# Kernel tuning notes

Hardware: AMD Instinct MI355X
Metric: run time of the kernel (lower is better)

The kernel has to match this reference:

```python
import jax, jax.numpy as jnp
import numpy as np

N_NODES = 100000
HEADS = 4
HEAD_DIM = 32  # hidden_channels // heads
NEG_SLOPE = 0.2


def gat_layer(x, W, a_src, a_dst, b, src, dst):
    # x: [N, Fin], W: [Fin, H*C], a_src/a_dst: [H, C], b: [H*C]
    N = x.shape[0]
    h = (x @ W).reshape(N, HEADS, HEAD_DIM)            # [N, H, C]
    alpha_s = jnp.einsum('nhc,hc->nh', h, a_src)       # [N, H]
    alpha_d = jnp.einsum('nhc,hc->nh', h, a_dst)       # [N, H]
    e = jax.nn.leaky_relu(alpha_s[src] + alpha_d[dst], NEG_SLOPE)  # [E, H]
    # segment softmax over edges grouped by destination node
    e_max = jax.ops.segment_max(e, dst, num_segments=N)           # [N, H]
    ex = jnp.exp(e - e_max[dst])                                   # [E, H]
    denom = jax.ops.segment_sum(ex, dst, num_segments=N)          # [N, H]
    alpha = ex / denom[dst]                                        # [E, H]
    msg = h[src] * alpha[:, :, None]                               # [E, H, C]
    out = jax.ops.segment_sum(msg, dst, num_segments=N)           # [N, H, C]
    return out.reshape(N, HEADS * HEAD_DIM) + b


def setup_inputs() -> dict:
    key = jax.random.key(0)
    ks = jax.random.split(key, 10)
    Fin, H, C = 128, HEADS, HEAD_DIM
    x = jax.random.normal(ks[0], (N_NODES, Fin), dtype=jnp.float32)
    edge_index = jax.random.randint(ks[1], (2, 1000000), 0, N_NODES, dtype=jnp.int64)
    s = 1.0 / np.sqrt(Fin)
    W1 = jax.random.normal(ks[2], (Fin, H * C), dtype=jnp.float32) * s
    a_src1 = jax.random.normal(ks[3], (H, C), dtype=jnp.float32) * 0.1
    a_dst1 = jax.random.normal(ks[4], (H, C), dtype=jnp.float32) * 0.1
    b1 = jnp.zeros((H * C,), dtype=jnp.float32)
    s2 = 1.0 / np.sqrt(H * C)
    W2 = jax.random.normal(ks[5], (H * C, H * C), dtype=jnp.float32) * s2
    a_src2 = jax.random.normal(ks[6], (H, C), dtype=jnp.float32) * 0.1
    a_dst2 = jax.random.normal(ks[7], (H, C), dtype=jnp.float32) * 0.1
    b2 = jnp.zeros((H * C,), dtype=jnp.float32)
    return {"x": x, "edge_index": edge_index, "W1": W1, "a_src1": a_src1,
            "a_dst1": a_dst1, "b1": b1, "W2": W2, "a_src2": a_src2,
            "a_dst2": a_dst2, "b2": b2}


def reference(x, edge_index, W1, a_src1, a_dst1, b1, W2, a_src2, a_dst2, b2):
    N = x.shape[0]
    # add self-loops (PyG add_self_loops=True)
    loop = jnp.arange(N, dtype=edge_index.dtype)
    src = jnp.concatenate([edge_index[0], loop])
    dst = jnp.concatenate([edge_index[1], loop])
    h = gat_layer(x, W1, a_src1, a_dst1, b1, src, dst)
    h = jax.nn.elu(h)
    h = gat_layer(h, W2, a_src2, a_dst2, b2, src, dst)
    h = jax.nn.elu(h)
    return h
```

## Files before the change

kernel.cpp:

```cpp
#include <hip/hip_runtime.h>
#include <math.h>

#define NHEADS 4
#define HDIM 32
#define F 128
#define ACH 8192

typedef __attribute__((ext_vector_type(8))) short bf16x8;
typedef __attribute__((ext_vector_type(4))) float f32x4;
typedef __attribute__((ext_vector_type(4))) unsigned u32x4;

__device__ __forceinline__ float lrelu(float v) { return v > 0.f ? v : 0.2f * v; }

__device__ __forceinline__ unsigned short cvt_bf16(float f) {
    unsigned u = __float_as_uint(f);
    u += 0x7fffu + ((u >> 16) & 1u);
    return (unsigned short)(u >> 16);
}

__global__ void k_packW2(const float* __restrict__ W1, const float* __restrict__ as1,
                         const float* __restrict__ ad1, const float* __restrict__ W2,
                         const float* __restrict__ as2, const float* __restrict__ ad2,
                         short* __restrict__ Wb) {
    int idx = blockIdx.x * 256 + threadIdx.x;
    if (idx >= 2 * 36 * 512) return;
    int half = idx >= 36 * 512;
    const float* W     = half ? W2 : W1;
    const float* a_src = half ? as2 : as1;
    const float* a_dst = half ? ad2 : ad1;
    int r = idx - half * 36 * 512;
    int j    = r & 7;
    int lane = (r >> 3) & 63;
    int frag = r >> 9;
    int kk = frag / 9, ct = frag % 9;
    int k = kk * 32 + (lane >> 4) * 8 + j;
    int col = lane & 15;
    float val;
    if (ct < 8) {
        val = W[k * F + ct * 16 + col];
    } else if (col < 8) {
        int head = col & 3;
        const float* av = (col < 4) ? a_src : a_dst;
        float sum = 0.f;
        #pragma unroll 8
        for (int c = 0; c < HDIM; ++c)
            sum += W[k * F + head * HDIM + c] * av[head * HDIM + c];
        val = sum;
    } else {
        val = 0.f;
    }
    Wb[idx] = (short)cvt_bf16(val);
}

template<bool ABF16>
__global__ __launch_bounds__(256) void k_gemm_mfma(
    const void* __restrict__ xv, const short* __restrict__ Wb,
    unsigned short* __restrict__ hbf, float* __restrict__ as_out,
    float* __restrict__ ad_out, int N)
{
    const int wid  = threadIdx.x >> 6;
    const int lane = threadIdx.x & 63;
    const int rowbase = blockIdx.x * 64 + wid * 16;
    const int row  = rowbase + (lane & 15);
    const int rowc = min(row, N - 1);
    const int col = lane & 15;

    f32x4 acc[9] = {};
    #pragma unroll
    for (int kk = 0; kk < 4; ++kk) {
        bf16x8 a;
        if constexpr (ABF16) {
            const unsigned short* xr =
                (const unsigned short*)xv + (size_t)rowc * F + (lane >> 4) * 8;
            a = *(const bf16x8*)(xr + kk * 32);
        } else {
            const float* xr = (const float*)xv + (size_t)rowc * F + (lane >> 4) * 8;
            float4 xa = *(const float4*)(xr + kk * 32);
            float4 xb = *(const float4*)(xr + kk * 32 + 4);
            a[0] = cvt_bf16(xa.x); a[1] = cvt_bf16(xa.y);
            a[2] = cvt_bf16(xa.z); a[3] = cvt_bf16(xa.w);
            a[4] = cvt_bf16(xb.x); a[5] = cvt_bf16(xb.y);
            a[6] = cvt_bf16(xb.z); a[7] = cvt_bf16(xb.w);
        }
        const bf16x8* bp = (const bf16x8*)(Wb + (size_t)(kk * 9) * 512 + lane * 8);
        #pragma unroll
        for (int ct = 0; ct < 9; ++ct) {
            bf16x8 b = bp[ct * 64];
            acc[ct] = __builtin_amdgcn_mfma_f32_16x16x32_bf16(a, b, acc[ct], 0, 0, 0);
        }
    }

    const int r0 = rowbase + (lane >> 4) * 4;
    #pragma unroll
    for (int i = 0; i < 4; ++i) {
        int r = r0 + i;
        if (r < N) {
            #pragma unroll
            for (int ct = 0; ct < 8; ++ct)
                __builtin_nontemporal_store(cvt_bf16(acc[ct][i]),
                                            &hbf[(size_t)r * F + ct * 16 + col]);
            if (col < 4)       as_out[r * NHEADS + col]     = acc[8][i];
            else if (col < 8)  ad_out[r * NHEADS + col - 4] = acc[8][i];
        }
    }
}


__global__ __launch_bounds__(512) void k_bhist(
    const int* __restrict__ src, const int* __restrict__ dst,
    int* __restrict__ bha, int nbuc, int E, int TOT)
{
    __shared__ int hist[512];
    int t = threadIdx.x;
    hist[t] = 0;
    __syncthreads();
    int base = blockIdx.x * ACH;
    for (int k = 0; k < ACH / 512; ++k) {
        int i = base + k * 512 + t;
        if (i < TOT) {
            int d = (i < E) ? dst[i] : (i - E);
            atomicAdd(&hist[d >> 8], 1);
        }
    }
    __syncthreads();
    if (t < nbuc) bha[(size_t)blockIdx.x * nbuc + t] = hist[t];
}

__global__ __launch_bounds__(256) void k_bscan1(
    int* __restrict__ bha, int* __restrict__ btot, int nbuc, int nab)
{
    int t = blockIdx.x * 256 + threadIdx.x;
    if (t >= nbuc) return;
    int run = 0;
    int j = 0;
    for (; j + 4 <= nab; j += 4) {
        int v0 = bha[(size_t)(j + 0) * nbuc + t];
        int v1 = bha[(size_t)(j + 1) * nbuc + t];
        int v2 = bha[(size_t)(j + 2) * nbuc + t];
        int v3 = bha[(size_t)(j + 3) * nbuc + t];
        bha[(size_t)(j + 0) * nbuc + t] = run; run += v0;
        bha[(size_t)(j + 1) * nbuc + t] = run; run += v1;
        bha[(size_t)(j + 2) * nbuc + t] = run; run += v2;
        bha[(size_t)(j + 3) * nbuc + t] = run; run += v3;
    }
    for (; j < nab; ++j) {
        int v = bha[(size_t)j * nbuc + t];
        bha[(size_t)j * nbuc + t] = run; run += v;
    }
    btot[t] = run;
}

__global__ __launch_bounds__(512) void k_bscan2(
    const int* __restrict__ btot, int* __restrict__ bbase, int nbuc)
{
    __shared__ int sh[512];
    int t = threadIdx.x;
    int v = (t < nbuc) ? btot[t] : 0;
    sh[t] = v;
    __syncthreads();
    for (int off = 1; off < 512; off <<= 1) {
        int u = (t >= off) ? sh[t - off] : 0;
        __syncthreads();
        sh[t] += u;
        __syncthreads();
    }
    if (t < nbuc) {
        bbase[t] = sh[t] - v;
        if (t == nbuc - 1) bbase[nbuc] = sh[t];
    }
}

__global__ __launch_bounds__(256) void k_bscan3(
    int* __restrict__ bha, const int* __restrict__ bbase, int nbuc, int total)
{
    int i = blockIdx.x * 256 + threadIdx.x;
    if (i < total) bha[i] += bbase[i % nbuc];
}

__global__ __launch_bounds__(512) void k_bscatter(
    const int* __restrict__ src, const int* __restrict__ dst,
    const int* __restrict__ bha, unsigned* __restrict__ epack,
    int nbuc, int E, int TOT)
{
    __shared__ int cur[512];
    int t = threadIdx.x;
    cur[t] = (t < nbuc) ? bha[(size_t)blockIdx.x * nbuc + t] : 0;
    __syncthreads();
    int base = blockIdx.x * ACH;
    for (int k = 0; k < ACH / 512; ++k) {
        int i = base + k * 512 + t;
        if (i < TOT) {
            int s, d;
            if (i < E) { s = src[i]; d = dst[i]; } else { s = d = i - E; }
            int pos = atomicAdd(&cur[d >> 8], 1);
            epack[pos] = ((unsigned)s << 8) | (unsigned)(d & 255);
        }
    }
}

__global__ __launch_bounds__(256) void k_bfinal(
    const unsigned* __restrict__ epack, const int* __restrict__ bbase,
    int* __restrict__ deg, int* __restrict__ rowptr, int* __restrict__ ssrc,
    int* __restrict__ bh, int N, int nbuc)
{
    __shared__ int hist[256];
    __shared__ int sh[256];
    __shared__ int cur[256];
    int t = threadIdx.x;
    hist[t] = 0;
    __syncthreads();
    int s0 = bbase[blockIdx.x], s1 = bbase[blockIdx.x + 1];
    for (int i = s0 + t; i < s1; i += 256)
        atomicAdd(&hist[epack[i] & 255u], 1);
    __syncthreads();
    int h = hist[t];
    sh[t] = h;
    __syncthreads();
    for (int off = 1; off < 256; off <<= 1) {
        int u = (t >= off) ? sh[t - off] : 0;
        __syncthreads();
        sh[t] += u;
        __syncthreads();
    }
    int node = blockIdx.x * 256 + t;
    int excl = s0 + sh[t] - h;
    cur[t] = excl;
    if (node < N) {
        deg[node] = h;
        rowptr[node] = excl;
        atomicAdd(&bh[(blockIdx.x >> 2) * 256 + min(h, 255)], 1);
    }
    if (node == 0) rowptr[N] = bbase[nbuc];
    __syncthreads();
    for (int i = s0 + t; i < s1; i += 256) {
        unsigned p = epack[i];
        int pos = atomicAdd(&cur[p & 255u], 1);
        ssrc[pos] = (int)(p >> 8);
    }
}

__global__ __launch_bounds__(256) void k_sort_off(int* __restrict__ bh, int nb)
{
    int t = threadIdx.x;
    int run = 0;
    for (int j = 0; j < nb; ++j) {
        int v = bh[j * 256 + t];
        bh[j * 256 + t] = run;
        run += v;
    }
    __shared__ int sh[256];
    int tot = run;
    sh[t] = tot;
    __syncthreads();
    for (int off = 1; off < 256; off <<= 1) {
        int u = (t >= off) ? sh[t - off] : 0;
        __syncthreads();
        sh[t] += u;
        __syncthreads();
    }
    int bucket_base = sh[t] - tot;
    for (int j = 0; j < nb; ++j)
        bh[j * 256 + t] += bucket_base;
}

__global__ __launch_bounds__(256) void k_sort_scatter(
    const int* __restrict__ deg, const int* __restrict__ bh,
    const int* __restrict__ rowptr, int4* __restrict__ ninfo, int N)
{
    __shared__ int cur[256];
    int t = threadIdx.x;
    cur[t] = bh[blockIdx.x * 256 + t];
    __syncthreads();
    int base = blockIdx.x * 1024;
    #pragma unroll
    for (int g = 0; g < 4; ++g) {
        int i = base + g * 256 + t;
        if (i < N) {
            int pos = atomicAdd(&cur[min(deg[i], 255)], 1);
            ninfo[pos] = make_int4(rowptr[i], rowptr[i + 1], i, 0);
        }
    }
}

template<bool OUTBF16>
__global__ __launch_bounds__(256) void k_aggregate(
    const int4* __restrict__ ninfo, const int* __restrict__ ssrc,
    const float* __restrict__ as, const float* __restrict__ ad,
    const unsigned short* __restrict__ hbf, const float* __restrict__ bias,
    void* __restrict__ outv, int N)
{
    int gi = (blockIdx.x * 256 + threadIdx.x) >> 4;
    if (gi >= N) return;
    const int4 ni   = ninfo[gi];
    const int start = ni.x, end = ni.y, node = ni.z;
    const int l16   = threadIdx.x & 15;
    const int hb    = l16 >> 2;
    const int c0    = l16 * 8;
    const float adB = ad[node * NHEADS + hb];

    float a0=0.f,a1=0.f,a2=0.f,a3=0.f,a4=0.f,a5=0.f,a6=0.f,a7=0.f;
    float dacc = 0.f;
    for (int base = start; base < end; base += 8) {
        int   sj[8];
        float fj[8];
        uint4 hj[8];
        #pragma unroll
        for (int j = 0; j < 8; ++j)
            sj[j] = ssrc[min(base + j, end - 1)];
        #pragma unroll
        for (int j = 0; j < 8; ++j)
            fj[j] = as[sj[j] * NHEADS + hb];
        #pragma unroll
        for (int j = 0; j < 8; ++j)
            hj[j] = *(const uint4*)(hbf + (size_t)sj[j] * F + c0);
        #pragma unroll
        for (int j = 0; j < 8; ++j) {
            float ex = (base + j < end) ? __expf(lrelu(fj[j] + adB)) : 0.f;
            dacc += ex;
            a0 = fmaf(ex, __uint_as_float(hj[j].x << 16),         a0);
            a1 = fmaf(ex, __uint_as_float(hj[j].x & 0xffff0000u), a1);
            a2 = fmaf(ex, __uint_as_float(hj[j].y << 16),         a2);
            a3 = fmaf(ex, __uint_as_float(hj[j].y & 0xffff0000u), a3);
            a4 = fmaf(ex, __uint_as_float(hj[j].z << 16),         a4);
            a5 = fmaf(ex, __uint_as_float(hj[j].z & 0xffff0000u), a5);
            a6 = fmaf(ex, __uint_as_float(hj[j].w << 16),         a6);
            a7 = fmaf(ex, __uint_as_float(hj[j].w & 0xffff0000u), a7);
        }
    }
    float inv = 1.f / dacc;
    float v[8] = {a0,a1,a2,a3,a4,a5,a6,a7};
    #pragma unroll
    for (int k = 0; k < 8; ++k) {
        float t = v[k] * inv + bias[c0 + k];
        v[k] = t > 0.f ? t : expm1f(t);
    }
    if (OUTBF16) {
        u32x4 o;
        o.x = (unsigned)cvt_bf16(v[0]) | ((unsigned)cvt_bf16(v[1]) << 16);
        o.y = (unsigned)cvt_bf16(v[2]) | ((unsigned)cvt_bf16(v[3]) << 16);
        o.z = (unsigned)cvt_bf16(v[4]) | ((unsigned)cvt_bf16(v[5]) << 16);
        o.w = (unsigned)cvt_bf16(v[6]) | ((unsigned)cvt_bf16(v[7]) << 16);
        __builtin_nontemporal_store(o,
            (u32x4*)((unsigned short*)outv + (size_t)node * F + c0));
    } else {
        f32x4 o0 = {v[0], v[1], v[2], v[3]};
        f32x4 o1 = {v[4], v[5], v[6], v[7]};
        float* op = (float*)outv + (size_t)node * F + c0;
        __builtin_nontemporal_store(o0, (f32x4*)op);
        __builtin_nontemporal_store(o1, (f32x4*)(op + 4));
    }
}

extern "C" void kernel_launch(void* const* d_in, const int* in_sizes, int n_in,
                              void* d_out, int out_size, void* d_ws, size_t ws_size,
                              hipStream_t stream)
{
    const float* x      = (const float*)d_in[0];
    const int*   eidx   = (const int*)d_in[1];
    const float* W1     = (const float*)d_in[2];
    const float* a_src1 = (const float*)d_in[3];
    const float* a_dst1 = (const float*)d_in[4];
    const float* b1     = (const float*)d_in[5];
    const float* W2     = (const float*)d_in[6];
    const float* a_src2 = (const float*)d_in[7];
    const float* a_dst2 = (const float*)d_in[8];
    const float* b2     = (const float*)d_in[9];

    const int N = in_sizes[0] / F;
    const int E = in_sizes[1] / 2;
    const int TOT = E + N;
    const int* src = eidx;
    const int* dst = eidx + E;

    const int nbuc = (N + 255) / 256;
    const int nab  = (TOT + ACH - 1) / ACH;
    const int nb   = (N + 1023) / 1024;

    unsigned* epack = (unsigned*)d_ws;
    unsigned short* hbf    = (unsigned short*)(epack + TOT);
    unsigned short* out1bf = hbf + (size_t)N * F;
    float* as = (float*)(out1bf + (size_t)N * F);
    float* ad = as + (size_t)N * NHEADS;
    int* deg    = (int*)(ad + (size_t)N * NHEADS);
    int* rowptr = deg + N;
    int* ssrc   = rowptr + N + 1;
    int4* ninfo = (int4*)(((uintptr_t)(ssrc + TOT) + 15) & ~(uintptr_t)15);
    int* bh     = (int*)(ninfo + N);
    int* bha    = bh + (size_t)nb * 256;
    int* btot   = bha + (size_t)nab * nbuc;
    int* bbase  = btot + nbuc;
    short* Wb1  = (short*)(((uintptr_t)(bbase + nbuc + 1) + 15) & ~(uintptr_t)15);

    const int gemmBlocks = (N + 63) / 64;
    const int aggBlocks  = (N + 15) / 16;

    k_packW2<<<144, 256, 0, stream>>>(W1, a_src1, a_dst1, W2, a_src2, a_dst2, Wb1);
    short* Wb2 = Wb1 + 36 * 512;

    k_bhist<<<nab, 512, 0, stream>>>(src, dst, bha, nbuc, E, TOT);
    k_bscan1<<<(nbuc + 255) / 256, 256, 0, stream>>>(bha, btot, nbuc, nab);
    k_bscan2<<<1, 512, 0, stream>>>(btot, bbase, nbuc);
    k_bscan3<<<(nab * nbuc + 255) / 256, 256, 0, stream>>>(bha, bbase, nbuc, nab * nbuc);
    k_bscatter<<<nab, 512, 0, stream>>>(src, dst, bha, epack, nbuc, E, TOT);
    (void)hipMemsetAsync(bh, 0, (size_t)nb * 256 * sizeof(int), stream);
    k_bfinal<<<nbuc, 256, 0, stream>>>(epack, bbase, deg, rowptr, ssrc, bh, N, nbuc);

    k_sort_off<<<1, 256, 0, stream>>>(bh, nb);
    k_sort_scatter<<<nb, 256, 0, stream>>>(deg, bh, rowptr, ninfo, N);

    k_gemm_mfma<false><<<gemmBlocks, 256, 0, stream>>>(x, Wb1, hbf, as, ad, N);
    k_aggregate<true><<<aggBlocks, 256, 0, stream>>>(ninfo, ssrc, as, ad, hbf, b1, out1bf, N);

    k_gemm_mfma<true><<<gemmBlocks, 256, 0, stream>>>(out1bf, Wb2, hbf, as, ad, N);
    k_aggregate<false><<<aggBlocks, 256, 0, stream>>>(ninfo, ssrc, as, ad, hbf, b2, d_out, N);
}
```

Before: 266.9 us.

## Fold scan-add into scatter, pre-scale logits by log2e, widen serial scan unroll

Removes the k_bscan3 launch by adding the bucket base offsets inside k_bscatter when its shared cursors are initialized. Attention logits are pre-multiplied by log2(e) in the GEMM epilogue so the aggregate can use exp2f instead of __expf. LeakyReLU is positively homogeneous, so this scaling leaves the result mathematically unchanged. The serial column scans in k_bscan1 and k_sort_off now unroll by 8 to keep more loads in flight, which costs some extra register use.

```diff
diff --git a/kernel.cpp b/kernel.cpp
--- a/kernel.cpp
+++ b/kernel.cpp
@@ -5,6 +5,7 @@
 #define HDIM 32
 #define F 128
 #define ACH 8192
+#define LOG2E 1.44269504088896340736f
 
 typedef __attribute__((ext_vector_type(8))) short bf16x8;
 typedef __attribute__((ext_vector_type(4))) float f32x4;
@@ -99,8 +100,8 @@
             for (int ct = 0; ct < 8; ++ct)
                 __builtin_nontemporal_store(cvt_bf16(acc[ct][i]),
                                             &hbf[(size_t)r * F + ct * 16 + col]);
-            if (col < 4)       as_out[r * NHEADS + col]     = acc[8][i];
-            else if (col < 8)  ad_out[r * NHEADS + col - 4] = acc[8][i];
+            if (col < 4)       as_out[r * NHEADS + col]     = acc[8][i] * LOG2E;
+            else if (col < 8)  ad_out[r * NHEADS + col - 4] = acc[8][i] * LOG2E;
         }
     }
 }
@@ -133,15 +134,12 @@
     if (t >= nbuc) return;
     int run = 0;
     int j = 0;
-    for (; j + 4 <= nab; j += 4) {
-        int v0 = bha[(size_t)(j + 0) * nbuc + t];
-        int v1 = bha[(size_t)(j + 1) * nbuc + t];
-        int v2 = bha[(size_t)(j + 2) * nbuc + t];
-        int v3 = bha[(size_t)(j + 3) * nbuc + t];
-        bha[(size_t)(j + 0) * nbuc + t] = run; run += v0;
-        bha[(size_t)(j + 1) * nbuc + t] = run; run += v1;
-        bha[(size_t)(j + 2) * nbuc + t] = run; run += v2;
-        bha[(size_t)(j + 3) * nbuc + t] = run; run += v3;
+    for (; j + 8 <= nab; j += 8) {
+        int v[8];
+        #pragma unroll
+        for (int u = 0; u < 8; ++u) v[u] = bha[(size_t)(j + u) * nbuc + t];
+        #pragma unroll
+        for (int u = 0; u < 8; ++u) { bha[(size_t)(j + u) * nbuc + t] = run; run += v[u]; }
     }
     for (; j < nab; ++j) {
         int v = bha[(size_t)j * nbuc + t];
@@ -170,21 +168,14 @@
     }
 }
 
-__global__ __launch_bounds__(256) void k_bscan3(
-    int* __restrict__ bha, const int* __restrict__ bbase, int nbuc, int total)
-{
-    int i = blockIdx.x * 256 + threadIdx.x;
-    if (i < total) bha[i] += bbase[i % nbuc];
-}
-
 __global__ __launch_bounds__(512) void k_bscatter(
     const int* __restrict__ src, const int* __restrict__ dst,
-    const int* __restrict__ bha, unsigned* __restrict__ epack,
-    int nbuc, int E, int TOT)
+    const int* __restrict__ bha, const int* __restrict__ bbase,
+    unsigned* __restrict__ epack, int nbuc, int E, int TOT)
 {
     __shared__ int cur[512];
     int t = threadIdx.x;
-    cur[t] = (t < nbuc) ? bha[(size_t)blockIdx.x * nbuc + t] : 0;
+    cur[t] = (t < nbuc) ? (bha[(size_t)blockIdx.x * nbuc + t] + bbase[t]) : 0;
     __syncthreads();
     int base = blockIdx.x * ACH;
     for (int k = 0; k < ACH / 512; ++k) {
@@ -243,7 +234,15 @@
 {
     int t = threadIdx.x;
     int run = 0;
-    for (int j = 0; j < nb; ++j) {
+    int j = 0;
+    for (; j + 8 <= nb; j += 8) {
+        int v[8];
+        #pragma unroll
+        for (int u = 0; u < 8; ++u) v[u] = bh[(j + u) * 256 + t];
+        #pragma unroll
+        for (int u = 0; u < 8; ++u) { bh[(j + u) * 256 + t] = run; run += v[u]; }
+    }
+    for (; j < nb; ++j) {
         int v = bh[j * 256 + t];
         bh[j * 256 + t] = run;
         run += v;
@@ -259,8 +258,8 @@
         __syncthreads();
     }
     int bucket_base = sh[t] - tot;
-    for (int j = 0; j < nb; ++j)
-        bh[j * 256 + t] += bucket_base;
+    for (int j2 = 0; j2 < nb; ++j2)
+        bh[j2 * 256 + t] += bucket_base;
 }
 
 __global__ __launch_bounds__(256) void k_sort_scatter(
@@ -315,7 +314,7 @@
             hj[j] = *(const uint4*)(hbf + (size_t)sj[j] * F + c0);
         #pragma unroll
         for (int j = 0; j < 8; ++j) {
-            float ex = (base + j < end) ? __expf(lrelu(fj[j] + adB)) : 0.f;
+            float ex = (base + j < end) ? exp2f(lrelu(fj[j] + adB)) : 0.f;
             dacc += ex;
             a0 = fmaf(ex, __uint_as_float(hj[j].x << 16),         a0);
             a1 = fmaf(ex, __uint_as_float(hj[j].x & 0xffff0000u), a1);
@@ -400,8 +399,7 @@
     k_bhist<<<nab, 512, 0, stream>>>(src, dst, bha, nbuc, E, TOT);
     k_bscan1<<<(nbuc + 255) / 256, 256, 0, stream>>>(bha, btot, nbuc, nab);
     k_bscan2<<<1, 512, 0, stream>>>(btot, bbase, nbuc);
-    k_bscan3<<<(nab * nbuc + 255) / 256, 256, 0, stream>>>(bha, bbase, nbuc, nab * nbuc);
-    k_bscatter<<<nab, 512, 0, stream>>>(src, dst, bha, epack, nbuc, E, TOT);
+    k_bscatter<<<nab, 512, 0, stream>>>(src, dst, bha, bbase, epack, nbuc, E, TOT);
     (void)hipMemsetAsync(bh, 0, (size_t)nb * 256 * sizeof(int), stream);
     k_bfinal<<<nbuc, 256, 0, stream>>>(epack, bbase, deg, rowptr, ssrc, bh, N, nbuc);
 
```

After: 245.0 us, median of 2. -8.2%, faster.
